# Kernel optimization log

Measured on AMD Instinct MI355X. Metric: run time of the kernel, lower is better.

## Reference

```python
import jax, jax.numpy as jnp
import numpy as np

B, N, E = 8, 2048, 1024


def setup_inputs() -> dict:
    key = jax.random.key(0)
    x = jax.random.normal(key, (B, N, E), dtype=jnp.float32)
    pos = jnp.ones((N - 1,), dtype=jnp.float32)
    zero = jnp.ones((1,), dtype=jnp.float32)
    neg = jnp.ones((N - 1,), dtype=jnp.float32)
    return {"x": x, "pos": pos, "zero": zero, "neg": neg}


def reference(x, pos, zero, neg):
    # x: [b, n, e]; Toeplitz matvec via circular FFT convolution of length 2n.
    b, n, e = x.shape
    # circulant kernel: [zero, pos[:n-1], zero, neg[-(n-1):]] -> length 2n
    a = jnp.concatenate([zero, pos[: n - 1], zero, neg[-(n - 1):]])
    # torch: fft(x, 2n, dim=1, norm='ortho')
    y = jnp.fft.fft(x, n=2 * n, axis=1, norm="ortho")  # [b, 2n, e] complex
    # torch: fft(a) with default ('backward') norm, i.e. unnormalized forward
    v = jnp.fft.fft(a)[None, :, None]                   # [1, 2n, 1]
    u = v * y
    out = jnp.fft.ifft(u, n=2 * n, axis=1, norm="ortho")[:, :n, :].real
    return out.astype(x.dtype)
```

## Files before the change

kernel.cpp:

```cpp
#include <hip/hip_runtime.h>
#include <stdint.h>


#define B_ 8
#define N_ 2048
#define NF 4096
#define E_ 1024

#define BUFSZ (NF + (NF >> 5))
__device__ __forceinline__ int P(int n) { return n + (n >> 5); }
#define PERM(r) ((((r) & 3) << 2) | ((r) >> 2))

__device__ __forceinline__ unsigned short f32_to_bf16_rne(float f) {
    union { float f; unsigned int u; } cv; cv.f = f;
    unsigned int u = cv.u;
    u += 0x7fffu + ((u >> 16) & 1u);
    return (unsigned short)(u >> 16);
}
__device__ __forceinline__ float bf16_to_f32(unsigned short u) {
    union { unsigned int u; float f; } cv; cv.u = ((unsigned int)u) << 16; return cv.f;
}
__device__ __forceinline__ void cmul(float& ar, float& ai, float br, float bi) {
    float t = ar * br - ai * bi; ai = ar * bi + ai * br; ar = t;
}

__device__ __forceinline__ void dft4(float& x0r, float& x0i, float& x1r, float& x1i,
                                     float& x2r, float& x2i, float& x3r, float& x3i,
                                     float sg) {
    float t0r = x0r + x2r, t0i = x0i + x2i;
    float t1r = x0r - x2r, t1i = x0i - x2i;
    float t2r = x1r + x3r, t2i = x1i + x3i;
    float t3r = x1r - x3r, t3i = x1i - x3i;
    x0r = t0r + t2r; x0i = t0i + t2i;
    x2r = t0r - t2r; x2i = t0i - t2i;
    x1r = t1r - sg * t3i; x1i = t1i + sg * t3r;
    x3r = t1r + sg * t3i; x3i = t1i - sg * t3r;
}

template<int SG>
__device__ __forceinline__ void dft16(float* xr, float* xi) {
    const float sg = (float)SG;
#pragma unroll
    for (int n0 = 0; n0 < 4; ++n0)
        dft4(xr[n0], xi[n0], xr[n0 + 4], xi[n0 + 4],
             xr[n0 + 8], xi[n0 + 8], xr[n0 + 12], xi[n0 + 12], sg);
    const float C1 = 0.923879532511286756f;
    const float S1 = 0.382683432365089772f;
    const float H  = 0.707106781186547524f;
    cmul(xr[5],  xi[5],  C1,  sg * S1);
    cmul(xr[9],  xi[9],  H,   sg * H);
    cmul(xr[13], xi[13], S1,  sg * C1);
    cmul(xr[6],  xi[6],  H,   sg * H);
    cmul(xr[10], xi[10], 0.f, sg);
    cmul(xr[14], xi[14], -H,  sg * H);
    cmul(xr[7],  xi[7],  S1,  sg * C1);
    cmul(xr[11], xi[11], -H,  sg * H);
    cmul(xr[15], xi[15], -C1, -sg * S1);
#pragma unroll
    for (int k1 = 0; k1 < 4; ++k1)
        dft4(xr[4 * k1], xi[4 * k1], xr[4 * k1 + 1], xi[4 * k1 + 1],
             xr[4 * k1 + 2], xi[4 * k1 + 2], xr[4 * k1 + 3], xi[4 * k1 + 3], sg);
}

template<int INV, int L>
__device__ __forceinline__ void fft_stage(float2* buf, const float2* __restrict__ tw2, int t) {
    constexpr int Lq = L / 16;
    int g = t / Lq;
    int j = t - g * Lq;
    int base = g * L + j;
    float xr[16], xi[16];
#pragma unroll
    for (int r = 0; r < 16; ++r) {
        float2 v = buf[P(base + r * Lq)];
        xr[r] = v.x; xi[r] = v.y;
    }
    float2 w1 = tw2[j * (NF / L)];
    float w1r = w1.x, w1i = INV ? -w1.y : w1.y;
    if (INV) {
        float wr = 1.f, wi = 0.f;
#pragma unroll
        for (int r = 1; r < 16; ++r) { cmul(wr, wi, w1r, w1i); cmul(xr[r], xi[r], wr, wi); }
        dft16<1>(xr, xi);
#pragma unroll
        for (int r = 0; r < 16; ++r) {
            float2 v; v.x = xr[PERM(r)]; v.y = xi[PERM(r)];
            buf[P(base + r * Lq)] = v;
        }
    } else {
        dft16<-1>(xr, xi);
        { float2 v; v.x = xr[0]; v.y = xi[0]; buf[P(base)] = v; }
        float wr = 1.f, wi = 0.f;
#pragma unroll
        for (int r = 1; r < 16; ++r) {
            cmul(wr, wi, w1r, w1i);
            float yr = xr[PERM(r)], yi = xi[PERM(r)];
            cmul(yr, yi, wr, wi);
            float2 v; v.x = yr; v.y = yi;
            buf[P(base + r * Lq)] = v;
        }
    }
}

__global__ __launch_bounds__(256) void build_tw(float2* tw2) {
    int k = blockIdx.x * 256 + threadIdx.x;
    double th = -6.283185307179586476925286766559 * (double)k / 4096.0;
    float2 v; v.x = (float)cos(th); v.y = (float)sin(th);
    tw2[k] = v;
}

__global__ __launch_bounds__(256) void build_V(const float* __restrict__ pos,
                                               const float* __restrict__ zero,
                                               const float* __restrict__ neg,
                                               const float2* __restrict__ tw2,
                                               float2* __restrict__ V2) {
    __shared__ float2 buf[BUFSZ];
    int t = threadIdx.x;
#pragma unroll
    for (int it = 0; it < 16; ++it) {
        int n = t + 256 * it;
        float v;
        if (n == 0) v = zero[0];
        else if (n < N_) v = pos[n - 1];
        else if (n == N_) v = zero[0];
        else v = neg[n - (N_ + 1)];
        float2 c; c.x = v; c.y = 0.f;
        buf[P(n)] = c;
    }
    __syncthreads();
    fft_stage<0, 4096>(buf, tw2, t); __syncthreads();
    fft_stage<0, 256>(buf, tw2, t);  __syncthreads();
    fft_stage<0, 16>(buf, tw2, t);   __syncthreads();
    const float s = 1.f / (float)NF;
#pragma unroll
    for (int it = 0; it < 16; ++it) {
        int n = t + 256 * it;
        float2 c = buf[P(n)];
        c.x *= s; c.y *= s;
        V2[n] = c;
    }
}

__global__ __launch_bounds__(256) void transpose_x(const float* __restrict__ x,
                                                   unsigned short* __restrict__ xT) {
    __shared__ float tile[64][66];
    int b  = blockIdx.z;
    int j0 = blockIdx.y * 64;
    int e0 = blockIdx.x * 64;
    int t  = threadIdx.x;

    int e4 = t & 15, jr = t >> 4;
#pragma unroll
    for (int it = 0; it < 4; ++it) {
        int j = jr + it * 16;
        const float4 v = *(const float4*)(x + ((size_t)(b * N_ + j0 + j) * E_) + e0 + e4 * 4);
        tile[e4 * 4 + 0][j] = v.x;
        tile[e4 * 4 + 1][j] = v.y;
        tile[e4 * 4 + 2][j] = v.z;
        tile[e4 * 4 + 3][j] = v.w;
    }
    __syncthreads();
    int j2 = (t & 31) * 2, er = t >> 5;
#pragma unroll
    for (int it = 0; it < 8; ++it) {
        int e = er + it * 8;
        float2 v = *(const float2*)&tile[e][j2];
        union { unsigned short s[2]; unsigned int u; } pk;
        pk.s[0] = f32_to_bf16_rne(v.x);
        pk.s[1] = f32_to_bf16_rne(v.y);
        *(unsigned int*)(xT + ((size_t)(b * E_ + e0 + e)) * N_ + j0 + j2) = pk.u;
    }
}

__global__ __launch_bounds__(256) void fft_conv(const unsigned short* __restrict__ xT,
                                                const float2* __restrict__ tw2,
                                                const float2* __restrict__ V2,
                                                float* __restrict__ out) {
    __shared__ float2 buf[BUFSZ];
    int t = threadIdx.x;
    int bid = blockIdx.x;
    int xcd = bid & 7;
    int q = bid >> 3;
    int b = q >> 6;
    int ep = xcd * 64 + (q & 63);
    int e0 = ep * 2;

    const unsigned short* r0 = xT + ((size_t)(b * E_ + e0)) * N_;
    uint4 u0 = ((const uint4*)r0)[t];
    uint4 u1 = ((const uint4*)(r0 + N_))[t];
    unsigned int a0[4] = { u0.x, u0.y, u0.z, u0.w };
    unsigned int a1[4] = { u1.x, u1.y, u1.z, u1.w };
#pragma unroll
    for (int i = 0; i < 4; ++i) {
        int n = 8 * t + 2 * i;
        float2 c0; c0.x = bf16_to_f32((unsigned short)(a0[i] & 0xffff));
        c0.y = bf16_to_f32((unsigned short)(a1[i] & 0xffff));
        buf[P(n)] = c0;
        float2 c1; c1.x = bf16_to_f32((unsigned short)(a0[i] >> 16));
        c1.y = bf16_to_f32((unsigned short)(a1[i] >> 16));
        buf[P(n + 1)] = c1;
    }
#pragma unroll
    for (int it = 0; it < 8; ++it) {
        int n = N_ + t + 256 * it;
        float2 z; z.x = 0.f; z.y = 0.f;
        buf[P(n)] = z;
    }
    __syncthreads();
    fft_stage<0, 4096>(buf, tw2, t); __syncthreads();
    fft_stage<0, 256>(buf, tw2, t);  __syncthreads();
    {
        int base = 16 * t;
        float xr[16], xi[16];
#pragma unroll
        for (int r = 0; r < 16; ++r) {
            float2 v = buf[P(base + r)];
            xr[r] = v.x; xi[r] = v.y;
        }
        dft16<-1>(xr, xi);
        float yr[16], yi[16];
#pragma unroll
        for (int r = 0; r < 16; ++r) {
            float2 vv = V2[base + r];
            float ar = xr[PERM(r)], ai = xi[PERM(r)];
            yr[r] = ar * vv.x - ai * vv.y;
            yi[r] = ar * vv.y + ai * vv.x;
        }
        dft16<1>(yr, yi);
#pragma unroll
        for (int r = 0; r < 16; ++r) {
            float2 v; v.x = yr[PERM(r)]; v.y = yi[PERM(r)];
            buf[P(base + r)] = v;
        }
    }
    __syncthreads();
    fft_stage<1, 256>(buf, tw2, t);  __syncthreads();
    fft_stage<1, 4096>(buf, tw2, t); __syncthreads();

    float* ob = out + ((size_t)b * N_) * E_ + e0;
#pragma unroll
    for (int it = 0; it < 8; ++it) {
        int k = t + 256 * it;
        float2 v = buf[P(k)];
        *(float2*)(ob + (size_t)k * E_) = v;
    }
}

__global__ __launch_bounds__(256) void naive_toep(const float* __restrict__ x,
                                                  const float* __restrict__ pos,
                                                  const float* __restrict__ zero,
                                                  const float* __restrict__ neg,
                                                  float* __restrict__ out) {
    int bid = blockIdx.x;
    int e   = (bid & 3) * 256 + threadIdx.x;
    int k   = (bid >> 2) & (N_ - 1);
    int b   = bid >> 13;
    float zv = zero[0];
    float acc = 0.f;
    const float* xb = x + (size_t)b * N_ * E_ + e;
    for (int j = 0; j < N_; ++j) {
        float c = (j < k) ? pos[k - j - 1] : (j == k) ? zv : neg[N_ - 1 - j + k];
        acc += c * xb[(size_t)j * E_];
    }
    out[((size_t)(b * N_ + k)) * E_ + e] = acc;
}

extern "C" void kernel_launch(void* const* d_in, const int* in_sizes, int n_in,
                              void* d_out, int out_size, void* d_ws, size_t ws_size,
                              hipStream_t stream) {
    const float* x    = (const float*)d_in[0];
    const float* pos  = (const float*)d_in[1];
    const float* zero = (const float*)d_in[2];
    const float* neg  = (const float*)d_in[3];
    float* out = (float*)d_out;

    const size_t needX = (size_t)B_ * E_ * N_ * sizeof(unsigned short);
    const size_t need  = needX + 2 * (size_t)NF * sizeof(float2);
    if (ws_size >= need) {
        unsigned short* xT = (unsigned short*)d_ws;
        float2* tw2 = (float2*)((char*)d_ws + needX);
        float2* V2  = tw2 + NF;
        build_tw<<<16, 256, 0, stream>>>(tw2);
        transpose_x<<<dim3(16, 32, 8), 256, 0, stream>>>(x, xT);
        build_V<<<1, 256, 0, stream>>>(pos, zero, neg, tw2, V2);
        fft_conv<<<4096, 256, 0, stream>>>(xT, tw2, V2, out);
    } else {
        naive_toep<<<65536, 256, 0, stream>>>(x, pos, zero, neg, out);
    }
}
```

Baseline: 201.8 us.

## Fuse load into first FFT stage, skip zero-pad work, precompute per-stage twiddles

The first forward radix-16 stage now reads the bf16 input straight from global memory into registers and uses a reduced first butterfly layer that exploits the zero upper half. This removes the shared-memory staging, the zero fill and one barrier. Per-stage twiddle tables (4096 and 256 entries) are precomputed, with __sincosf replacing double cos/sin, so the in-kernel twiddle recurrence goes away. The last inverse stage computes only the outputs that are kept and writes them directly to global, skipping the final shared-memory round trip. The cost is extra twiddle loads from global/cache, plus some precision loss from the fast sincos.

```diff
diff --git a/kernel.cpp b/kernel.cpp
--- a/kernel.cpp
+++ b/kernel.cpp
@@ -22,6 +22,9 @@
 }
 __device__ __forceinline__ void cmul(float& ar, float& ai, float br, float bi) {
     float t = ar * br - ai * bi; ai = ar * bi + ai * br; ar = t;
+}
+__device__ __forceinline__ void cmulc(float& ar, float& ai, float br, float bi) {
+    float t = ar * br + ai * bi; ai = ai * br - ar * bi; ar = t;
 }
 
 __device__ __forceinline__ void dft4(float& x0r, float& x0i, float& x1r, float& x1i,
@@ -38,12 +41,28 @@
 }
 
 template<int SG>
-__device__ __forceinline__ void dft16(float* xr, float* xi) {
+__device__ __forceinline__ void dft16_layer1(float* xr, float* xi) {
     const float sg = (float)SG;
 #pragma unroll
     for (int n0 = 0; n0 < 4; ++n0)
         dft4(xr[n0], xi[n0], xr[n0 + 4], xi[n0 + 4],
              xr[n0 + 8], xi[n0 + 8], xr[n0 + 12], xi[n0 + 12], sg);
+}
+template<int SG>
+__device__ __forceinline__ void dft16_layer1_pad(float* xr, float* xi) {
+    const float sg = (float)SG;
+#pragma unroll
+    for (int n0 = 0; n0 < 4; ++n0) {
+        float ar = xr[n0], ai = xi[n0], br = xr[n0 + 4], bi = xi[n0 + 4];
+        xr[n0]      = ar + br;       xi[n0]      = ai + bi;
+        xr[n0 + 4]  = ar - sg * bi;  xi[n0 + 4]  = ai + sg * br;
+        xr[n0 + 8]  = ar - br;       xi[n0 + 8]  = ai - bi;
+        xr[n0 + 12] = ar + sg * bi;  xi[n0 + 12] = ai - sg * br;
+    }
+}
+template<int SG>
+__device__ __forceinline__ void dft16_twiddle(float* xr, float* xi) {
+    const float sg = (float)SG;
     const float C1 = 0.923879532511286756f;
     const float S1 = 0.382683432365089772f;
     const float H  = 0.707106781186547524f;
@@ -56,10 +75,20 @@
     cmul(xr[7],  xi[7],  S1,  sg * C1);
     cmul(xr[11], xi[11], -H,  sg * H);
     cmul(xr[15], xi[15], -C1, -sg * S1);
+}
+template<int SG>
+__device__ __forceinline__ void dft16_layer2(float* xr, float* xi) {
+    const float sg = (float)SG;
 #pragma unroll
     for (int k1 = 0; k1 < 4; ++k1)
         dft4(xr[4 * k1], xi[4 * k1], xr[4 * k1 + 1], xi[4 * k1 + 1],
              xr[4 * k1 + 2], xi[4 * k1 + 2], xr[4 * k1 + 3], xi[4 * k1 + 3], sg);
+}
+template<int SG>
+__device__ __forceinline__ void dft16(float* xr, float* xi) {
+    dft16_layer1<SG>(xr, xi);
+    dft16_twiddle<SG>(xr, xi);
+    dft16_layer2<SG>(xr, xi);
 }
 
 template<int INV, int L>
@@ -101,11 +130,26 @@
     }
 }
 
-__global__ __launch_bounds__(256) void build_tw(float2* tw2) {
-    int k = blockIdx.x * 256 + threadIdx.x;
-    double th = -6.283185307179586476925286766559 * (double)k / 4096.0;
-    float2 v; v.x = (float)cos(th); v.y = (float)sin(th);
-    tw2[k] = v;
+__global__ __launch_bounds__(256) void build_tw(float2* tw2, float2* tw4096, float2* tw256) {
+    const float TPI = -6.28318530717958647692f;
+    int blk = blockIdx.x, t = threadIdx.x;
+    if (blk < 16) {
+        int k = blk * 256 + t;
+        float s, c;
+        __sincosf(TPI * (float)k * (1.f / 4096.f), &s, &c);
+        float2 v; v.x = c; v.y = s;
+        tw2[k] = v;
+        int rj = (blk * t) & (NF - 1);
+        __sincosf(TPI * (float)rj * (1.f / 4096.f), &s, &c);
+        float2 w; w.x = c; w.y = s;
+        tw4096[blk * 256 + t] = w;
+    } else {
+        int r = t >> 4, j = t & 15;
+        float s, c;
+        __sincosf(TPI * (float)(r * j) * (1.f / 256.f), &s, &c);
+        float2 v; v.x = c; v.y = s;
+        tw256[t] = v;
+    }
 }
 
 __global__ __launch_bounds__(256) void build_V(const float* __restrict__ pos,
@@ -172,7 +216,8 @@
 }
 
 __global__ __launch_bounds__(256) void fft_conv(const unsigned short* __restrict__ xT,
-                                                const float2* __restrict__ tw2,
+                                                const float2* __restrict__ tw4096,
+                                                const float2* __restrict__ tw256,
                                                 const float2* __restrict__ V2,
                                                 float* __restrict__ out) {
     __shared__ float2 buf[BUFSZ];
@@ -181,67 +226,130 @@
     int xcd = bid & 7;
     int q = bid >> 3;
     int b = q >> 6;
-    int ep = xcd * 64 + (q & 63);
-    int e0 = ep * 2;
+    int e0 = (xcd * 64 + (q & 63)) * 2;
 
     const unsigned short* r0 = xT + ((size_t)(b * E_ + e0)) * N_;
-    uint4 u0 = ((const uint4*)r0)[t];
-    uint4 u1 = ((const uint4*)(r0 + N_))[t];
-    unsigned int a0[4] = { u0.x, u0.y, u0.z, u0.w };
-    unsigned int a1[4] = { u1.x, u1.y, u1.z, u1.w };
-#pragma unroll
-    for (int i = 0; i < 4; ++i) {
-        int n = 8 * t + 2 * i;
-        float2 c0; c0.x = bf16_to_f32((unsigned short)(a0[i] & 0xffff));
-        c0.y = bf16_to_f32((unsigned short)(a1[i] & 0xffff));
-        buf[P(n)] = c0;
-        float2 c1; c1.x = bf16_to_f32((unsigned short)(a0[i] >> 16));
-        c1.y = bf16_to_f32((unsigned short)(a1[i] >> 16));
-        buf[P(n + 1)] = c1;
-    }
-#pragma unroll
-    for (int it = 0; it < 8; ++it) {
-        int n = N_ + t + 256 * it;
-        float2 z; z.x = 0.f; z.y = 0.f;
-        buf[P(n)] = z;
-    }
-    __syncthreads();
-    fft_stage<0, 4096>(buf, tw2, t); __syncthreads();
-    fft_stage<0, 256>(buf, tw2, t);  __syncthreads();
+    const unsigned short* r1 = r0 + N_;
+
+    float xr[16], xi[16];
+
+#pragma unroll
+    for (int r = 0; r < 8; ++r) {
+        int n = t + 256 * r;
+        xr[r] = bf16_to_f32(r0[n]);
+        xi[r] = bf16_to_f32(r1[n]);
+    }
+#pragma unroll
+    for (int r = 8; r < 16; ++r) { xr[r] = 0.f; xi[r] = 0.f; }
+    dft16_layer1_pad<-1>(xr, xi);
+    dft16_twiddle<-1>(xr, xi);
+    dft16_layer2<-1>(xr, xi);
+    { float2 v; v.x = xr[0]; v.y = xi[0]; buf[P(t)] = v; }
+#pragma unroll
+    for (int r = 1; r < 16; ++r) {
+        float2 w = tw4096[r * 256 + t];
+        float yr = xr[PERM(r)], yi = xi[PERM(r)];
+        cmul(yr, yi, w.x, w.y);
+        float2 v; v.x = yr; v.y = yi;
+        buf[P(t + 256 * r)] = v;
+    }
+    __syncthreads();
+
+    int g = t >> 4, j = t & 15;
+    int base = g * 256 + j;
+#pragma unroll
+    for (int r = 0; r < 16; ++r) {
+        float2 v = buf[P(base + 16 * r)];
+        xr[r] = v.x; xi[r] = v.y;
+    }
+    dft16<-1>(xr, xi);
+    { float2 v; v.x = xr[0]; v.y = xi[0]; buf[P(base)] = v; }
+#pragma unroll
+    for (int r = 1; r < 16; ++r) {
+        float2 w = tw256[r * 16 + j];
+        float yr = xr[PERM(r)], yi = xi[PERM(r)];
+        cmul(yr, yi, w.x, w.y);
+        float2 v; v.x = yr; v.y = yi;
+        buf[P(base + 16 * r)] = v;
+    }
+    __syncthreads();
+
     {
-        int base = 16 * t;
-        float xr[16], xi[16];
+        int mb = 16 * t;
 #pragma unroll
         for (int r = 0; r < 16; ++r) {
-            float2 v = buf[P(base + r)];
+            float2 v = buf[P(mb + r)];
             xr[r] = v.x; xi[r] = v.y;
         }
         dft16<-1>(xr, xi);
-        float yr[16], yi[16];
+        float yr2[16], yi2[16];
+        const float4* Vv = (const float4*)(V2 + mb);
+#pragma unroll
+        for (int h = 0; h < 8; ++h) {
+            float4 vv = Vv[h];
+            int r = 2 * h;
+            float ar = xr[PERM(r)], ai = xi[PERM(r)];
+            yr2[r] = ar * vv.x - ai * vv.y;
+            yi2[r] = ar * vv.y + ai * vv.x;
+            r = 2 * h + 1;
+            ar = xr[PERM(r)]; ai = xi[PERM(r)];
+            yr2[r] = ar * vv.z - ai * vv.w;
+            yi2[r] = ar * vv.w + ai * vv.z;
+        }
+        dft16<1>(yr2, yi2);
 #pragma unroll
         for (int r = 0; r < 16; ++r) {
-            float2 vv = V2[base + r];
-            float ar = xr[PERM(r)], ai = xi[PERM(r)];
-            yr[r] = ar * vv.x - ai * vv.y;
-            yi[r] = ar * vv.y + ai * vv.x;
-        }
-        dft16<1>(yr, yi);
-#pragma unroll
-        for (int r = 0; r < 16; ++r) {
-            float2 v; v.x = yr[PERM(r)]; v.y = yi[PERM(r)];
-            buf[P(base + r)] = v;
-        }
-    }
-    __syncthreads();
-    fft_stage<1, 256>(buf, tw2, t);  __syncthreads();
-    fft_stage<1, 4096>(buf, tw2, t); __syncthreads();
-
+            float2 v; v.x = yr2[PERM(r)]; v.y = yi2[PERM(r)];
+            buf[P(mb + r)] = v;
+        }
+    }
+    __syncthreads();
+
+#pragma unroll
+    for (int r = 0; r < 16; ++r) {
+        float2 v = buf[P(base + 16 * r)];
+        xr[r] = v.x; xi[r] = v.y;
+    }
+#pragma unroll
+    for (int r = 1; r < 16; ++r) {
+        float2 w = tw256[r * 16 + j];
+        cmulc(xr[r], xi[r], w.x, w.y);
+    }
+    dft16<1>(xr, xi);
+#pragma unroll
+    for (int r = 0; r < 16; ++r) {
+        float2 v; v.x = xr[PERM(r)]; v.y = xi[PERM(r)];
+        buf[P(base + 16 * r)] = v;
+    }
+    __syncthreads();
+
+#pragma unroll
+    for (int r = 0; r < 16; ++r) {
+        float2 v = buf[P(t + 256 * r)];
+        xr[r] = v.x; xi[r] = v.y;
+    }
+#pragma unroll
+    for (int r = 1; r < 16; ++r) {
+        float2 w = tw4096[r * 256 + t];
+        cmulc(xr[r], xi[r], w.x, w.y);
+    }
+    dft16_layer1<1>(xr, xi);
+    dft16_twiddle<1>(xr, xi);
     float* ob = out + ((size_t)b * N_) * E_ + e0;
 #pragma unroll
-    for (int it = 0; it < 8; ++it) {
-        int k = t + 256 * it;
-        float2 v = buf[P(k)];
-        *(float2*)(ob + (size_t)k * E_) = v;
+    for (int k1 = 0; k1 < 4; ++k1) {
+        float a0r = xr[4 * k1],     a0i = xi[4 * k1];
+        float a1r = xr[4 * k1 + 1], a1i = xi[4 * k1 + 1];
+        float a2r = xr[4 * k1 + 2], a2i = xi[4 * k1 + 2];
+        float a3r = xr[4 * k1 + 3], a3i = xi[4 * k1 + 3];
+        float t0r = a0r + a2r, t0i = a0i + a2i;
+        float t1r = a0r - a2r, t1i = a0i - a2i;
+        float t2r = a1r + a3r, t2i = a1i + a3i;
+        float t3r = a1r - a3r, t3i = a1i - a3i;
+        float2 v0; v0.x = t0r + t2r; v0.y = t0i + t2i;
+        float2 v1; v1.x = t1r - t3i; v1.y = t1i + t3r;
+        *(float2*)(ob + (size_t)(t + 256 * k1) * E_)       = v0;
+        *(float2*)(ob + (size_t)(t + 256 * (k1 + 4)) * E_) = v1;
     }
 }
 
@@ -257,9 +365,9 @@
     float zv = zero[0];
     float acc = 0.f;
     const float* xb = x + (size_t)b * N_ * E_ + e;
-    for (int j = 0; j < N_; ++j) {
-        float c = (j < k) ? pos[k - j - 1] : (j == k) ? zv : neg[N_ - 1 - j + k];
-        acc += c * xb[(size_t)j * E_];
+    for (int jj = 0; jj < N_; ++jj) {
+        float c = (jj < k) ? pos[k - jj - 1] : (jj == k) ? zv : neg[N_ - 1 - jj + k];
+        acc += c * xb[(size_t)jj * E_];
     }
     out[((size_t)(b * N_ + k)) * E_ + e] = acc;
 }
@@ -274,15 +382,17 @@
     float* out = (float*)d_out;
 
     const size_t needX = (size_t)B_ * E_ * N_ * sizeof(unsigned short);
-    const size_t need  = needX + 2 * (size_t)NF * sizeof(float2);
+    const size_t need  = needX + (3 * (size_t)NF + 256) * sizeof(float2);
     if (ws_size >= need) {
         unsigned short* xT = (unsigned short*)d_ws;
-        float2* tw2 = (float2*)((char*)d_ws + needX);
-        float2* V2  = tw2 + NF;
-        build_tw<<<16, 256, 0, stream>>>(tw2);
+        float2* tw2    = (float2*)((char*)d_ws + needX);
+        float2* V2     = tw2 + NF;
+        float2* tw4096 = V2 + NF;
+        float2* tw256  = tw4096 + NF;
+        build_tw<<<17, 256, 0, stream>>>(tw2, tw4096, tw256);
         transpose_x<<<dim3(16, 32, 8), 256, 0, stream>>>(x, xT);
         build_V<<<1, 256, 0, stream>>>(pos, zero, neg, tw2, V2);
-        fft_conv<<<4096, 256, 0, stream>>>(xT, tw2, V2, out);
+        fft_conv<<<4096, 256, 0, stream>>>(xT, tw4096, tw256, V2, out);
     } else {
         naive_toep<<<65536, 256, 0, stream>>>(x, pos, zero, neg, out);
     }
```

After: 205.9 us. 1.02x slower.
